# Performance work log

Measured on AMD Instinct MI355X. Metric: run time of the kernel, lower is better.

## Reference

```python
import jax, jax.numpy as jnp
import numpy as np

N = 65536   # base nodes
M = 65536   # union local nodes
E = 1048576 # base edges
EL = 1048576 # local edges
K = 131072  # membership entries
F = 128     # in_channels
H = 128     # hidden_dim
L = 2       # num_layers
OUT = 2
ALPHA = 0.9


def setup_inputs() -> dict:
    key = jax.random.key(0)
    ks = jax.random.split(key, 16)
    s = 1.0 / np.sqrt(H)
    return {
        "x": jax.random.normal(ks[0], (N, F), jnp.float32),
        "edge_index": jax.random.randint(ks[1], (2, E), 0, N, jnp.int64 if jax.config.jax_enable_x64 else jnp.int32),
        "edge_weight": jax.random.uniform(ks[2], (E,), jnp.float32),
        "local_x0": jax.random.normal(ks[3], (M, F), jnp.float32),
        "copy2orig": jax.random.randint(ks[4], (M,), 0, N),
        "local_adj_index": jax.random.randint(ks[5], (2, EL), 0, M),
        "local_adj_value": jax.random.uniform(ks[6], (EL,), jnp.float32),
        "memb_idx": jax.random.randint(ks[7], (K,), 0, M),
        "memb_gid": jax.random.randint(ks[8], (K,), 0, 64),
        "B": 64,
        "Wb_in": jax.random.normal(ks[9], (F, H), jnp.float32) * s,
        "bb_in": jnp.zeros((H,), jnp.float32),
        "Wl_in": jax.random.normal(ks[10], (F, H), jnp.float32) * s,
        "bl_in": jnp.zeros((H,), jnp.float32),
        "W_base": jax.random.normal(ks[11], (L, H, H), jnp.float32) * s,
        "b_base": jnp.zeros((L, H), jnp.float32),
        "W_local": jax.random.normal(ks[12], (L, H, H), jnp.float32) * s,
        "b_local": jnp.zeros((L, H), jnp.float32),
        "Wp": jax.random.normal(ks[13], (H, OUT), jnp.float32) * s,
        "bp": jnp.zeros((OUT,), jnp.float32),
    }


def reference(x, edge_index, edge_weight, local_x0, copy2orig, local_adj_index,
              local_adj_value, memb_idx, memb_gid, B, Wb_in, bb_in, Wl_in, bl_in,
              W_base, b_base, W_local, b_local, Wp, bp):
    n = x.shape[0]
    m = local_x0.shape[0]
    # input projections (dropout is identity in eval mode)
    base_x = jax.nn.relu(x @ Wb_in + bb_in)
    local_x = jax.nn.relu(local_x0 @ Wl_in + bl_in)
    src, dst = edge_index[0], edge_index[1]
    lsrc, ldst = local_adj_index[0], local_adj_index[1]
    for l in range(W_base.shape[0]):
        # base graph propagation: normalized-adjacency spmm then linear+relu
        base_agg = jax.ops.segment_sum(base_x[src] * edge_weight[:, None], dst, num_segments=n)
        base_x = jax.nn.relu(base_agg @ W_base[l] + b_base[l])
        # local union-graph propagation + alpha-mix with base features via copy2orig
        local_agg = jax.ops.segment_sum(local_x[lsrc] * local_adj_value[:, None], ldst, num_segments=m)
        mix = ALPHA * local_agg + (1.0 - ALPHA) * base_x[copy2orig]
        local_x = jax.nn.relu(mix @ W_local[l] + b_local[l])
    # scatter-mean pooling by membership (fused sum + count)
    sub = jax.ops.segment_sum(local_x[memb_idx], memb_gid, num_segments=B)
    cnt = jax.ops.segment_sum(jnp.ones((memb_gid.shape[0], 1), local_x.dtype), memb_gid, num_segments=B)
    sub = sub / jnp.maximum(cnt, 1.0)
    return sub @ Wp + bp
```

## Files before the change

kernel.cpp:

```cpp
#include <hip/hip_runtime.h>

typedef __attribute__((ext_vector_type(8))) short bfrag;
typedef __attribute__((ext_vector_type(4))) float ffrag;

__device__ __forceinline__ ushort f2bf(float f) {
    union { float f; unsigned u; } v{f};
    unsigned r = v.u + 0x7fff + ((v.u >> 16) & 1);
    return (ushort)(r >> 16);
}
__device__ __forceinline__ float bf2f(ushort u) {
    union { unsigned u; float f; } v{(unsigned)u << 16};
    return v.f;
}
__device__ __forceinline__ float bflo(unsigned u) {
    union { unsigned u; float f; } v{u << 16};
    return v.f;
}
__device__ __forceinline__ float bfhi(unsigned u) {
    union { unsigned u; float f; } v{u & 0xffff0000u};
    return v.f;
}

#define WDEC (1.f / 65535.f)

#define NB 512
#define BSH 7
#define CH2 2048
#define CAP 4608
#define PCAP 2432


__global__ __launch_bounds__(256) void wprep_zero(const float* __restrict__ Wb_in, const float* __restrict__ Wl_in,
                                                  const float* __restrict__ W_base, const float* __restrict__ W_local,
                                                  ushort* __restrict__ out,
                                                  int* __restrict__ bs_cur, int* __restrict__ ls_cur,
                                                  int* __restrict__ p_cur, int* __restrict__ psum) {
    const int bid = blockIdx.x;
    const int t = threadIdx.x;
    if (bid < 384) {
        int idx = bid * 256 + t;
        int mat = idx >> 14;
        int i = idx & 16383;
        int nn = i >> 7, kk = i & 127;
        const float* src;
        switch (mat) {
            case 0: src = Wb_in; break;
            case 1: src = Wl_in; break;
            case 2: src = W_base; break;
            case 3: src = W_base + 16384; break;
            case 4: src = W_local; break;
            default: src = W_local + 16384; break;
        }
        out[(size_t)mat * 16384 + i] = f2bf(src[kk * 128 + nn]);
    } else {
        int i = (bid - 384) * 256 + t;
        if (i < 512) { bs_cur[i] = i * CAP; ls_cur[i] = i * CAP; }
        if (i < 64) p_cur[i] = i * PCAP;
        psum[i] = 0;
    }
}


__global__ __launch_bounds__(512) void b1p(const int* __restrict__ b_src, const int* __restrict__ b_dst,
                                           const float* __restrict__ b_w, int* __restrict__ b_cur,
                                           int2* __restrict__ b_staged,
                                           const int* __restrict__ l_src, const int* __restrict__ l_dst,
                                           const float* __restrict__ l_w, int* __restrict__ l_cur,
                                           int2* __restrict__ l_staged,
                                           const int* __restrict__ memb_idx, const int* __restrict__ memb_gid,
                                           int* __restrict__ p_cursor, int* __restrict__ p_sorted) {
    __shared__ int cnt_s[NB], base_l[NB], base_g[NB], curs[NB];
    __shared__ int wtot[8];
    __shared__ int2 stage[CH2];
    __shared__ ushort bb[CH2];
    __shared__ int lhist[64], lbase[64], loff[1024];
    const int t = threadIdx.x;
    const int bid = blockIdx.x;
    if (bid < 1024) {
        const int g = bid >> 9;
        const int* src = g ? l_src : b_src;
        const int* dst = g ? l_dst : b_dst;
        const float* w = g ? l_w : b_w;
        int* bcursor = g ? l_cur : b_cur;
        int2* staged = g ? l_staged : b_staged;
        const int base = (bid & 511) * CH2;
        cnt_s[t] = 0;
        __syncthreads();
#pragma unroll
        for (int u = 0; u < CH2 / 512; ++u) {
            int b = ((unsigned)dst[base + u * 512 + t]) >> BSH;
            atomicAdd(&cnt_s[b], 1);
        }
        __syncthreads();
        int v = cnt_s[t];
        int lane = t & 63, wid = t >> 6;
        int inc = v;
        for (int o = 1; o < 64; o <<= 1) { int x = __shfl_up(inc, o); if (lane >= o) inc += x; }
        if (lane == 63) wtot[wid] = inc;
        __syncthreads();
        int wpre = 0;
#pragma unroll
        for (int j = 0; j < 8; ++j) if (j < wid) wpre += wtot[j];
        int excl = wpre + inc - v;
        base_l[t] = excl;
        curs[t] = excl;
        base_g[t] = atomicAdd(&bcursor[t], v);
        __syncthreads();
#pragma unroll
        for (int u = 0; u < CH2 / 512; ++u) {
            int e = base + u * 512 + t;
            int d = dst[e];
            int b = ((unsigned)d) >> BSH;
            int p = atomicAdd(&curs[b], 1);
            stage[p] = make_int2((src[e] & 0xffff) | ((d & 127) << 16), __float_as_int(w[e]));
            bb[p] = (ushort)b;
        }
        __syncthreads();
        for (int i = t; i < CH2; i += 512) {
            int b = bb[i];
            staged[base_g[b] + (i - base_l[b])] = stage[i];
        }
    } else {
        if (t < 64) lhist[t] = 0;
        __syncthreads();
        const int base = (bid - 1024) * 1024;
        int g[2], ix[2];
#pragma unroll
        for (int u = 0; u < 2; ++u) {
            int e = base + u * 512 + t;
            g[u] = memb_gid[e];
            ix[u] = memb_idx[e];
            loff[u * 512 + t] = atomicAdd(&lhist[g[u]], 1);
        }
        __syncthreads();
        if (t < 64) lbase[t] = atomicAdd(&p_cursor[t], lhist[t]);
        __syncthreads();
#pragma unroll
        for (int u = 0; u < 2; ++u) {
            int pos = lbase[g[u]] + loff[u * 512 + t];
            p_sorted[pos] = ix[u];
        }
    }
}

#define ASTRIDE 136


__global__ __launch_bounds__(256) void b2g(const int* __restrict__ b_cur, const int2* __restrict__ b_staged,
                                           int2* __restrict__ b_rng, int* __restrict__ b_edges,
                                           const int* __restrict__ l_cur, const int2* __restrict__ l_staged,
                                           int2* __restrict__ l_rng, int* __restrict__ l_edges,
                                           const float* __restrict__ Ab, const float* __restrict__ Al,
                                           const ushort* __restrict__ Wt,
                                           const float* __restrict__ biasb, const float* __restrict__ biasl,
                                           ushort* __restrict__ Yb, ushort* __restrict__ Yl) {
    __shared__ __align__(16) char smem[52224];
    __shared__ int cnt[256], curs[256], wt4[4];
    const int t = threadIdx.x;
    const int bid = blockIdx.x;
    if (bid < 1024) {
        const int g = bid >> 9;
        const int b = bid & 511;
        const int* bcur = g ? l_cur : b_cur;
        const int2* staged = g ? l_staged : b_staged;
        int2* rng = g ? l_rng : b_rng;
        int* edges = g ? l_edges : b_edges;
        const int s0 = b * CAP;
        int len = bcur[b] - s0;
        if (len > CAP) len = CAP;
        cnt[t] = 0;
        __syncthreads();
        int* seg = (int*)smem;
        int* ord = (int*)(smem + CAP * 4);
        unsigned char* segd = (unsigned char*)(smem + CAP * 8);
        for (int i = t; i < len; i += 256) {
            int2 se = staged[s0 + i];
            int key = (((se.x >> 16) & 127) << 1) | ((se.x >> 15) & 1);
            unsigned wq = (unsigned)(__int_as_float(se.y) * 65535.f + 0.5f);
            seg[i] = (int)(((unsigned)se.x & 0xffffu) | (wq << 16));
            segd[i] = (unsigned char)key;
            atomicAdd(&cnt[key], 1);
        }
        __syncthreads();
        int v = cnt[t];
        int lane = t & 63, wid = t >> 6;
        int inc = v;
        for (int o = 1; o < 64; o <<= 1) { int x = __shfl_up(inc, o); if (lane >= o) inc += x; }
        if (lane == 63) wt4[wid] = inc;
        __syncthreads();
        int wpre = 0;
#pragma unroll
        for (int j = 0; j < 4; ++j) if (j < wid) wpre += wt4[j];
        int excl = wpre + inc - v;
        curs[t] = excl;
        if (!(t & 1))
            rng[b * 128 + (t >> 1)] = make_int2(s0 + excl, s0 + excl + v + cnt[t + 1]);
        __syncthreads();
        for (int i = t; i < len; i += 256) {
            int p = atomicAdd(&curs[segd[i]], 1);
            ord[p] = seg[i];
        }
        __syncthreads();
        for (int i = t; i < len; i += 256)
            edges[s0 + i] = ord[i];
    } else {
        ushort* As = (ushort*)smem;
        ushort* Bs = (ushort*)(smem + 64 * ASTRIDE * 2);
        const int bid2 = bid - 1024;
        const int g = bid2 >> 10;
        const float* A = g ? Al : Ab;
        const ushort* W = Wt + (size_t)g * 16384;
        const float* bias = g ? biasl : biasb;
        ushort* Y = g ? Yl : Yb;
        const int r0 = (bid2 & 1023) * 64;

#pragma unroll
        for (int p = 0; p < 8; ++p) {
            int c = p * 256 + t;
            int row = c >> 5, o4 = (c & 31) * 4;
            float4 v = *(const float4*)(A + (size_t)(r0 + row) * 128 + o4);
            ushort4 u;
            u.x = f2bf(v.x); u.y = f2bf(v.y); u.z = f2bf(v.z); u.w = f2bf(v.w);
            *(ushort4*)&As[row * ASTRIDE + o4] = u;
        }
#pragma unroll
        for (int p = 0; p < 8; ++p) {
            int c = p * 256 + t;
            int n = c >> 4, o8 = (c & 15) * 8;
            *(uint4*)&Bs[n * ASTRIDE + o8] = *(const uint4*)(W + n * 128 + o8);
        }
        __syncthreads();

        const int lane = t & 63;
        const int w = t >> 6;
        const int wm = (w & 1) * 32;
        const int wn = (w >> 1) * 64;
        const int q = lane >> 4;
        const int l16 = lane & 15;

        ffrag acc[2][4];
#pragma unroll
        for (int mt = 0; mt < 2; ++mt)
#pragma unroll
            for (int nt = 0; nt < 4; ++nt) acc[mt][nt] = (ffrag){0.f, 0.f, 0.f, 0.f};

#pragma unroll
        for (int kc = 0; kc < 4; ++kc) {
            bfrag a[2], b[4];
#pragma unroll
            for (int mt = 0; mt < 2; ++mt)
                a[mt] = *(const bfrag*)&As[(wm + mt * 16 + l16) * ASTRIDE + kc * 32 + q * 8];
#pragma unroll
            for (int nt = 0; nt < 4; ++nt)
                b[nt] = *(const bfrag*)&Bs[(wn + nt * 16 + l16) * ASTRIDE + kc * 32 + q * 8];
#pragma unroll
            for (int mt = 0; mt < 2; ++mt)
#pragma unroll
                for (int nt = 0; nt < 4; ++nt)
                    acc[mt][nt] = __builtin_amdgcn_mfma_f32_16x16x32_bf16(a[mt], b[nt], acc[mt][nt], 0, 0, 0);
        }

        float bias_v[4];
#pragma unroll
        for (int nt = 0; nt < 4; ++nt) bias_v[nt] = bias[wn + nt * 16 + l16];
#pragma unroll
        for (int mt = 0; mt < 2; ++mt)
#pragma unroll
            for (int nt = 0; nt < 4; ++nt)
#pragma unroll
                for (int r = 0; r < 4; ++r) {
                    int row = r0 + wm + mt * 16 + q * 4 + r;
                    int col = wn + nt * 16 + l16;
                    float v = fmaxf(acc[mt][nt][r] + bias_v[nt], 0.f);
                    Y[(size_t)row * 128 + col] = f2bf(v);
                }
    }
}


template <bool MIX>
__global__ __launch_bounds__(256) void gemm_layer(const ushort* __restrict__ A, const ushort* __restrict__ A2,
                                                  const int* __restrict__ ridx,
                                                  const ushort* __restrict__ Wt, const float* __restrict__ bias,
                                                  ushort* __restrict__ Y) {
    __shared__ ushort As[64 * ASTRIDE];
    __shared__ ushort Bs[128 * ASTRIDE];
    const int tid = threadIdx.x;
    const int r0 = blockIdx.x * 64;

#pragma unroll
    for (int p = 0; p < 4; ++p) {
        int c = p * 256 + tid;
        int row = c >> 4, o8 = (c & 15) * 8;
        uint4 v = *(const uint4*)(A + (size_t)(r0 + row) * 128 + o8);
        if (MIX) {
            int rr = ridx[r0 + row];
            uint4 v2 = *(const uint4*)(A2 + (size_t)rr * 128 + o8);
            uint4 o;
            float x0, x1;
            x0 = 0.9f * bflo(v.x) + 0.1f * bflo(v2.x);
            x1 = 0.9f * bfhi(v.x) + 0.1f * bfhi(v2.x);
            o.x = (unsigned)f2bf(x0) | ((unsigned)f2bf(x1) << 16);
            x0 = 0.9f * bflo(v.y) + 0.1f * bflo(v2.y);
            x1 = 0.9f * bfhi(v.y) + 0.1f * bfhi(v2.y);
            o.y = (unsigned)f2bf(x0) | ((unsigned)f2bf(x1) << 16);
            x0 = 0.9f * bflo(v.z) + 0.1f * bflo(v2.z);
            x1 = 0.9f * bfhi(v.z) + 0.1f * bfhi(v2.z);
            o.z = (unsigned)f2bf(x0) | ((unsigned)f2bf(x1) << 16);
            x0 = 0.9f * bflo(v.w) + 0.1f * bflo(v2.w);
            x1 = 0.9f * bfhi(v.w) + 0.1f * bfhi(v2.w);
            o.w = (unsigned)f2bf(x0) | ((unsigned)f2bf(x1) << 16);
            v = o;
        }
        *(uint4*)&As[row * ASTRIDE + o8] = v;
    }
#pragma unroll
    for (int p = 0; p < 8; ++p) {
        int c = p * 256 + tid;
        int n = c >> 4, o8 = (c & 15) * 8;
        *(uint4*)&Bs[n * ASTRIDE + o8] = *(const uint4*)(Wt + n * 128 + o8);
    }
    __syncthreads();

    const int lane = tid & 63;
    const int w = tid >> 6;
    const int wm = (w & 1) * 32;
    const int wn = (w >> 1) * 64;
    const int q = lane >> 4;
    const int l16 = lane & 15;

    ffrag acc[2][4];
#pragma unroll
    for (int mt = 0; mt < 2; ++mt)
#pragma unroll
        for (int nt = 0; nt < 4; ++nt) acc[mt][nt] = (ffrag){0.f, 0.f, 0.f, 0.f};

#pragma unroll
    for (int kc = 0; kc < 4; ++kc) {
        bfrag a[2], b[4];
#pragma unroll
        for (int mt = 0; mt < 2; ++mt)
            a[mt] = *(const bfrag*)&As[(wm + mt * 16 + l16) * ASTRIDE + kc * 32 + q * 8];
#pragma unroll
        for (int nt = 0; nt < 4; ++nt)
            b[nt] = *(const bfrag*)&Bs[(wn + nt * 16 + l16) * ASTRIDE + kc * 32 + q * 8];
#pragma unroll
        for (int mt = 0; mt < 2; ++mt)
#pragma unroll
            for (int nt = 0; nt < 4; ++nt)
                acc[mt][nt] = __builtin_amdgcn_mfma_f32_16x16x32_bf16(a[mt], b[nt], acc[mt][nt], 0, 0, 0);
    }

    float bias_v[4];
#pragma unroll
    for (int nt = 0; nt < 4; ++nt) bias_v[nt] = bias[wn + nt * 16 + l16];
#pragma unroll
    for (int mt = 0; mt < 2; ++mt)
#pragma unroll
        for (int nt = 0; nt < 4; ++nt)
#pragma unroll
            for (int r = 0; r < 4; ++r) {
                int row = r0 + wm + mt * 16 + q * 4 + r;
                int col = wn + nt * 16 + l16;
                float v = fmaxf(acc[mt][nt][r] + bias_v[nt], 0.f);
                Y[(size_t)row * 128 + col] = f2bf(v);
            }
}


__global__ __launch_bounds__(256) void spmm2(const int2* __restrict__ bs_rng, const int* __restrict__ bs_edges,
                                             const ushort* __restrict__ Xb, ushort* __restrict__ Yb,
                                             const int2* __restrict__ ls_rng, const int* __restrict__ ls_edges,
                                             const ushort* __restrict__ Xl, ushort* __restrict__ Yl) {
    const int g = blockIdx.x & 1;
    const int2* rng = g ? ls_rng : bs_rng;
    const int* edges = g ? ls_edges : bs_edges;
    const ushort* X = g ? Xl : Xb;
    ushort* Y = g ? Yl : Yb;
    int node = (((blockIdx.x >> 1) * 256) + threadIdx.x) >> 5;
    int lane = threadIdx.x & 31;
    int2 r = rng[node];
    int s0 = r.x;
    int s1 = r.y;
    const int f = lane * 4;
    float a0 = 0.f, a1 = 0.f, a2 = 0.f, a3 = 0.f;
    int e = s0;
    for (; e < s1 && (e & 3); ++e) {
        unsigned pe = (unsigned)edges[e];
        float w = (float)(pe >> 16) * WDEC;
        ushort4 v = *(const ushort4*)(X + ((size_t)(pe & 0xffffu) << 7) + f);
        a0 += w * bf2f(v.x); a1 += w * bf2f(v.y); a2 += w * bf2f(v.z); a3 += w * bf2f(v.w);
    }
    for (; e + 8 <= s1; e += 8) {
        int4 pA = *(const int4*)(edges + e);
        int4 pB = *(const int4*)(edges + e + 4);
        ushort4 v0 = *(const ushort4*)(X + ((size_t)((unsigned)pA.x & 0xffffu) << 7) + f);
        ushort4 v1 = *(const ushort4*)(X + ((size_t)((unsigned)pA.y & 0xffffu) << 7) + f);
        ushort4 v2 = *(const ushort4*)(X + ((size_t)((unsigned)pA.z & 0xffffu) << 7) + f);
        ushort4 v3 = *(const ushort4*)(X + ((size_t)((unsigned)pA.w & 0xffffu) << 7) + f);
        ushort4 v4 = *(const ushort4*)(X + ((size_t)((unsigned)pB.x & 0xffffu) << 7) + f);
        ushort4 v5 = *(const ushort4*)(X + ((size_t)((unsigned)pB.y & 0xffffu) << 7) + f);
        ushort4 v6 = *(const ushort4*)(X + ((size_t)((unsigned)pB.z & 0xffffu) << 7) + f);
        ushort4 v7 = *(const ushort4*)(X + ((size_t)((unsigned)pB.w & 0xffffu) << 7) + f);
        float w0 = (float)((unsigned)pA.x >> 16) * WDEC;
        float w1 = (float)((unsigned)pA.y >> 16) * WDEC;
        float w2 = (float)((unsigned)pA.z >> 16) * WDEC;
        float w3 = (float)((unsigned)pA.w >> 16) * WDEC;
        float w4 = (float)((unsigned)pB.x >> 16) * WDEC;
        float w5 = (float)((unsigned)pB.y >> 16) * WDEC;
        float w6 = (float)((unsigned)pB.z >> 16) * WDEC;
        float w7 = (float)((unsigned)pB.w >> 16) * WDEC;
        a0 += w0 * bf2f(v0.x) + w1 * bf2f(v1.x) + w2 * bf2f(v2.x) + w3 * bf2f(v3.x)
            + w4 * bf2f(v4.x) + w5 * bf2f(v5.x) + w6 * bf2f(v6.x) + w7 * bf2f(v7.x);
        a1 += w0 * bf2f(v0.y) + w1 * bf2f(v1.y) + w2 * bf2f(v2.y) + w3 * bf2f(v3.y)
            + w4 * bf2f(v4.y) + w5 * bf2f(v5.y) + w6 * bf2f(v6.y) + w7 * bf2f(v7.y);
        a2 += w0 * bf2f(v0.z) + w1 * bf2f(v1.z) + w2 * bf2f(v2.z) + w3 * bf2f(v3.z)
            + w4 * bf2f(v4.z) + w5 * bf2f(v5.z) + w6 * bf2f(v6.z) + w7 * bf2f(v7.z);
        a3 += w0 * bf2f(v0.w) + w1 * bf2f(v1.w) + w2 * bf2f(v2.w) + w3 * bf2f(v3.w)
            + w4 * bf2f(v4.w) + w5 * bf2f(v5.w) + w6 * bf2f(v6.w) + w7 * bf2f(v7.w);
    }
    for (; e + 4 <= s1; e += 4) {
        int4 pA = *(const int4*)(edges + e);
        ushort4 v0 = *(const ushort4*)(X + ((size_t)((unsigned)pA.x & 0xffffu) << 7) + f);
        ushort4 v1 = *(const ushort4*)(X + ((size_t)((unsigned)pA.y & 0xffffu) << 7) + f);
        ushort4 v2 = *(const ushort4*)(X + ((size_t)((unsigned)pA.z & 0xffffu) << 7) + f);
        ushort4 v3 = *(const ushort4*)(X + ((size_t)((unsigned)pA.w & 0xffffu) << 7) + f);
        float w0 = (float)((unsigned)pA.x >> 16) * WDEC;
        float w1 = (float)((unsigned)pA.y >> 16) * WDEC;
        float w2 = (float)((unsigned)pA.z >> 16) * WDEC;
        float w3 = (float)((unsigned)pA.w >> 16) * WDEC;
        a0 += w0 * bf2f(v0.x) + w1 * bf2f(v1.x) + w2 * bf2f(v2.x) + w3 * bf2f(v3.x);
        a1 += w0 * bf2f(v0.y) + w1 * bf2f(v1.y) + w2 * bf2f(v2.y) + w3 * bf2f(v3.y);
        a2 += w0 * bf2f(v0.z) + w1 * bf2f(v1.z) + w2 * bf2f(v2.z) + w3 * bf2f(v3.z);
        a3 += w0 * bf2f(v0.w) + w1 * bf2f(v1.w) + w2 * bf2f(v2.w) + w3 * bf2f(v3.w);
    }
    for (; e < s1; ++e) {
        unsigned pe = (unsigned)edges[e];
        float w = (float)(pe >> 16) * WDEC;
        ushort4 v = *(const ushort4*)(X + ((size_t)(pe & 0xffffu) << 7) + f);
        a0 += w * bf2f(v.x); a1 += w * bf2f(v.y); a2 += w * bf2f(v.z); a3 += w * bf2f(v.w);
    }
    ushort4 o;
    o.x = f2bf(a0);
    o.y = f2bf(a1);
    o.z = f2bf(a2);
    o.w = f2bf(a3);
    *(ushort4*)(Y + (size_t)node * 128 + f) = o;
}


__global__ __launch_bounds__(256) void pool_accum(const int* __restrict__ p_cur, const int* __restrict__ sorted_idx,
                                                  const ushort* __restrict__ X, float* __restrict__ gsum) {
    const int g = blockIdx.x >> 5;
    const int sgm = blockIdx.x & 31;
    const int gs = g * PCAP;
    const int cnt = p_cur[g] - gs;
    const int e_begin = gs + ((cnt * sgm) >> 5);
    const int e_end = gs + ((cnt * (sgm + 1)) >> 5);
    const int t = threadIdx.x;
    const int fp = t & 63;
    const int sub = t >> 6;
    float ax = 0.f, ay = 0.f;
#pragma unroll 4
    for (int e = e_begin + sub; e < e_end; e += 4) {
        int idx = sorted_idx[e];
        ushort2 u = *(const ushort2*)(X + (size_t)idx * 128 + fp * 2);
        ax += bf2f(u.x);
        ay += bf2f(u.y);
    }
    __shared__ float sx[256], sy[256];
    sx[t] = ax;
    sy[t] = ay;
    __syncthreads();
    if (t < 64) {
        atomicAdd(&gsum[g * 128 + fp * 2 + 0], sx[t] + sx[t + 64] + sx[t + 128] + sx[t + 192]);
        atomicAdd(&gsum[g * 128 + fp * 2 + 1], sy[t] + sy[t + 64] + sy[t + 128] + sy[t + 192]);
    }
}


__global__ __launch_bounds__(128) void final_kernel(const float* __restrict__ gsum, const int* __restrict__ p_cur,
                                                    const float* __restrict__ Wp, const float* __restrict__ bp,
                                                    float* __restrict__ out) {
    int t = threadIdx.x;
    int g = t >> 1;
    int o = t & 1;
    float cnt = (float)(p_cur[g] - g * PCAP);
    float inv = 1.f / fmaxf(cnt, 1.f);
    float acc = bp[o];
    for (int f = 0; f < 128; ++f) acc += gsum[g * 128 + f] * inv * Wp[f * 2 + o];
    out[g * 2 + o] = acc;
}


extern "C" void kernel_launch(void* const* d_in, const int* in_sizes, int n_in,
                              void* d_out, int out_size, void* d_ws, size_t ws_size,
                              hipStream_t stream) {
    const float* x              = (const float*)d_in[0];
    const int*   edge_index     = (const int*)d_in[1];
    const float* edge_weight    = (const float*)d_in[2];
    const float* local_x0       = (const float*)d_in[3];
    const int*   copy2orig      = (const int*)d_in[4];
    const int*   local_adj_idx  = (const int*)d_in[5];
    const float* local_adj_val  = (const float*)d_in[6];
    const int*   memb_idx       = (const int*)d_in[7];
    const int*   memb_gid       = (const int*)d_in[8];
    const float* Wb_in          = (const float*)d_in[10];
    const float* bb_in          = (const float*)d_in[11];
    const float* Wl_in          = (const float*)d_in[12];
    const float* bl_in          = (const float*)d_in[13];
    const float* W_base         = (const float*)d_in[14];
    const float* b_base         = (const float*)d_in[15];
    const float* W_local        = (const float*)d_in[16];
    const float* b_local        = (const float*)d_in[17];
    const float* Wp             = (const float*)d_in[18];
    const float* bp             = (const float*)d_in[19];
    float* out = (float*)d_out;

    constexpr int N = 65536, M = 65536, E = 1048576, EL = 1048576, K = 131072, H = 128;

    char* wsb = (char*)d_ws;
    size_t off = 0;
    auto alloc = [&](size_t bytes) -> char* {
        char* p = wsb + off;
        off += (bytes + 255) & ~(size_t)255;
        return p;
    };
    int2*   bs_rng   = (int2*)alloc((size_t)N * 8);
    int*    bs_edges = (int*)alloc((size_t)NB * CAP * 4);
    int2*   bs_stage = (int2*)alloc((size_t)NB * CAP * 8);
    int*    bs_cur   = (int*)alloc(NB * 4);
    int2*   ls_rng   = (int2*)alloc((size_t)M * 8);
    int*    ls_edges = (int*)alloc((size_t)NB * CAP * 4);
    int2*   ls_stage = (int2*)alloc((size_t)NB * CAP * 8);
    int*    ls_cur   = (int*)alloc(NB * 4);
    ushort* bufA     = (ushort*)alloc((size_t)N * H * 2);
    ushort* bufB     = (ushort*)alloc((size_t)M * H * 2);
    ushort* bufC     = (ushort*)alloc((size_t)N * H * 2);
    ushort* bufD     = (ushort*)alloc((size_t)M * H * 2);
    ushort* wt       = (ushort*)alloc((size_t)6 * 16384 * 2);
    int*    p_cursor = (int*)alloc(64 * 4);
    int*    p_sorted = (int*)alloc((size_t)64 * PCAP * 4);
    float*  pool_sum = (float*)alloc(64 * 128 * 4);

    const int* b_src = edge_index;
    const int* b_dst = edge_index + E;
    const int* l_src = local_adj_idx;
    const int* l_dst = local_adj_idx + EL;

    wprep_zero<<<416, 256, 0, stream>>>(Wb_in, Wl_in, W_base, W_local, wt,
                                        bs_cur, ls_cur, p_cursor, (int*)pool_sum);

    b1p<<<1152, 512, 0, stream>>>(b_src, b_dst, edge_weight, bs_cur, bs_stage,
                                  l_src, l_dst, local_adj_val, ls_cur, ls_stage,
                                  memb_idx, memb_gid, p_cursor, p_sorted);

    b2g<<<3072, 256, 0, stream>>>(bs_cur, bs_stage, bs_rng, bs_edges,
                                  ls_cur, ls_stage, ls_rng, ls_edges,
                                  x, local_x0, wt, bb_in, bl_in, bufA, bufB);

    for (int l = 0; l < 2; ++l) {
        spmm2<<<16384, 256, 0, stream>>>(bs_rng, bs_edges, bufA, bufC,
                                         ls_rng, ls_edges, bufB, bufD);
        gemm_layer<false><<<N / 64, 256, 0, stream>>>(bufC, nullptr, nullptr,
                                                      wt + (size_t)(2 + l) * 16384, b_base + (size_t)l * H, bufA);
        gemm_layer<true><<<M / 64, 256, 0, stream>>>(bufD, bufA, copy2orig,
                                                     wt + (size_t)(4 + l) * 16384, b_local + (size_t)l * H, bufB);
    }

    pool_accum<<<64 * 32, 256, 0, stream>>>(p_cursor, p_sorted, bufB, pool_sum);
    final_kernel<<<1, 128, 0, stream>>>(pool_sum, p_cursor, Wp, bp, out);
}
```

Measured before the change: 392.9 us.

## Pack staged edges into 32-bit words with 9-bit weights; prefetch edge indices in SpMM

Edge weights are now quantized to 9 bits at the staging pass, so each staged edge fits in one 32-bit word holding the source id, the low destination bits and the weight. This halves staging traffic and simplifies the per-bucket sort to 128 keys with one range per row instead of paired keys. The SpMM 8-edge loop is software-pipelined, loading the next edge-index vectors before processing the current ones, with padding added to the edge buffers to allow the lookahead reads. Quantizing weights to 9 bits lowers precision noticeably compared with the previous 16-bit encoding and may cost accuracy.

```diff
diff --git a/kernel.cpp b/kernel.cpp
--- a/kernel.cpp
+++ b/kernel.cpp
@@ -21,7 +21,7 @@
     return v.f;
 }
 
-#define WDEC (1.f / 65535.f)
+#define WDEC (1.f / 511.f)
 
 #define NB 512
 #define BSH 7
@@ -63,15 +63,15 @@
 
 __global__ __launch_bounds__(512) void b1p(const int* __restrict__ b_src, const int* __restrict__ b_dst,
                                            const float* __restrict__ b_w, int* __restrict__ b_cur,
-                                           int2* __restrict__ b_staged,
+                                           int* __restrict__ b_staged,
                                            const int* __restrict__ l_src, const int* __restrict__ l_dst,
                                            const float* __restrict__ l_w, int* __restrict__ l_cur,
-                                           int2* __restrict__ l_staged,
+                                           int* __restrict__ l_staged,
                                            const int* __restrict__ memb_idx, const int* __restrict__ memb_gid,
                                            int* __restrict__ p_cursor, int* __restrict__ p_sorted) {
     __shared__ int cnt_s[NB], base_l[NB], base_g[NB], curs[NB];
     __shared__ int wtot[8];
-    __shared__ int2 stage[CH2];
+    __shared__ int stage[CH2];
     __shared__ ushort bb[CH2];
     __shared__ int lhist[64], lbase[64], loff[1024];
     const int t = threadIdx.x;
@@ -82,7 +82,7 @@
         const int* dst = g ? l_dst : b_dst;
         const float* w = g ? l_w : b_w;
         int* bcursor = g ? l_cur : b_cur;
-        int2* staged = g ? l_staged : b_staged;
+        int* staged = g ? l_staged : b_staged;
         const int base = (bid & 511) * CH2;
         cnt_s[t] = 0;
         __syncthreads();
@@ -112,7 +112,8 @@
             int d = dst[e];
             int b = ((unsigned)d) >> BSH;
             int p = atomicAdd(&curs[b], 1);
-            stage[p] = make_int2((src[e] & 0xffff) | ((d & 127) << 16), __float_as_int(w[e]));
+            unsigned wq = (unsigned)(w[e] * 511.f + 0.5f);
+            stage[p] = (int)(((unsigned)src[e] & 0xffffu) | ((unsigned)(d & 127) << 16) | (wq << 23));
             bb[p] = (ushort)b;
         }
         __syncthreads();
@@ -146,55 +147,55 @@
 #define ASTRIDE 136
 
 
-__global__ __launch_bounds__(256) void b2g(const int* __restrict__ b_cur, const int2* __restrict__ b_staged,
+__global__ __launch_bounds__(256) void b2g(const int* __restrict__ b_cur, const int* __restrict__ b_staged,
                                            int2* __restrict__ b_rng, int* __restrict__ b_edges,
-                                           const int* __restrict__ l_cur, const int2* __restrict__ l_staged,
+                                           const int* __restrict__ l_cur, const int* __restrict__ l_staged,
                                            int2* __restrict__ l_rng, int* __restrict__ l_edges,
                                            const float* __restrict__ Ab, const float* __restrict__ Al,
                                            const ushort* __restrict__ Wt,
                                            const float* __restrict__ biasb, const float* __restrict__ biasl,
                                            ushort* __restrict__ Yb, ushort* __restrict__ Yl) {
     __shared__ __align__(16) char smem[52224];
-    __shared__ int cnt[256], curs[256], wt4[4];
+    __shared__ int cnt[128], curs[128], wt2[2];
     const int t = threadIdx.x;
     const int bid = blockIdx.x;
     if (bid < 1024) {
         const int g = bid >> 9;
         const int b = bid & 511;
         const int* bcur = g ? l_cur : b_cur;
-        const int2* staged = g ? l_staged : b_staged;
+        const int* staged = g ? l_staged : b_staged;
         int2* rng = g ? l_rng : b_rng;
         int* edges = g ? l_edges : b_edges;
         const int s0 = b * CAP;
         int len = bcur[b] - s0;
         if (len > CAP) len = CAP;
-        cnt[t] = 0;
+        if (t < 128) cnt[t] = 0;
         __syncthreads();
         int* seg = (int*)smem;
         int* ord = (int*)(smem + CAP * 4);
         unsigned char* segd = (unsigned char*)(smem + CAP * 8);
         for (int i = t; i < len; i += 256) {
-            int2 se = staged[s0 + i];
-            int key = (((se.x >> 16) & 127) << 1) | ((se.x >> 15) & 1);
-            unsigned wq = (unsigned)(__int_as_float(se.y) * 65535.f + 0.5f);
-            seg[i] = (int)(((unsigned)se.x & 0xffffu) | (wq << 16));
-            segd[i] = (unsigned char)key;
-            atomicAdd(&cnt[key], 1);
-        }
-        __syncthreads();
-        int v = cnt[t];
-        int lane = t & 63, wid = t >> 6;
-        int inc = v;
-        for (int o = 1; o < 64; o <<= 1) { int x = __shfl_up(inc, o); if (lane >= o) inc += x; }
-        if (lane == 63) wt4[wid] = inc;
-        __syncthreads();
-        int wpre = 0;
-#pragma unroll
-        for (int j = 0; j < 4; ++j) if (j < wid) wpre += wt4[j];
-        int excl = wpre + inc - v;
-        curs[t] = excl;
-        if (!(t & 1))
-            rng[b * 128 + (t >> 1)] = make_int2(s0 + excl, s0 + excl + v + cnt[t + 1]);
+            int v = staged[s0 + i];
+            int dl = (v >> 16) & 127;
+            unsigned wq = ((unsigned)v) >> 23;
+            seg[i] = (int)(((unsigned)v & 0xffffu) | (wq << 16));
+            segd[i] = (unsigned char)dl;
+            atomicAdd(&cnt[dl], 1);
+        }
+        __syncthreads();
+        int v = 0, inc = 0;
+        if (t < 128) {
+            v = cnt[t];
+            inc = v;
+            for (int o = 1; o < 64; o <<= 1) { int x = __shfl_up(inc, o); if ((t & 63) >= o) inc += x; }
+            if ((t & 63) == 63) wt2[t >> 6] = inc;
+        }
+        __syncthreads();
+        if (t < 128) {
+            int excl = inc - v + (t >= 64 ? wt2[0] : 0);
+            curs[t] = excl;
+            rng[b * 128 + t] = make_int2(s0 + excl, s0 + excl + v);
+        }
         __syncthreads();
         for (int i = t; i < len; i += 256) {
             int p = atomicAdd(&curs[segd[i]], 1);
@@ -368,6 +369,34 @@
 }
 
 
+#define PROC8(pA, pB)                                                                          \
+    {                                                                                          \
+        ushort4 v0 = *(const ushort4*)(X + ((size_t)((unsigned)pA.x & 0xffffu) << 7) + f);     \
+        ushort4 v1 = *(const ushort4*)(X + ((size_t)((unsigned)pA.y & 0xffffu) << 7) + f);     \
+        ushort4 v2 = *(const ushort4*)(X + ((size_t)((unsigned)pA.z & 0xffffu) << 7) + f);     \
+        ushort4 v3 = *(const ushort4*)(X + ((size_t)((unsigned)pA.w & 0xffffu) << 7) + f);     \
+        ushort4 v4 = *(const ushort4*)(X + ((size_t)((unsigned)pB.x & 0xffffu) << 7) + f);     \
+        ushort4 v5 = *(const ushort4*)(X + ((size_t)((unsigned)pB.y & 0xffffu) << 7) + f);     \
+        ushort4 v6 = *(const ushort4*)(X + ((size_t)((unsigned)pB.z & 0xffffu) << 7) + f);     \
+        ushort4 v7 = *(const ushort4*)(X + ((size_t)((unsigned)pB.w & 0xffffu) << 7) + f);     \
+        float w0 = (float)((unsigned)pA.x >> 16) * WDEC;                                       \
+        float w1 = (float)((unsigned)pA.y >> 16) * WDEC;                                       \
+        float w2 = (float)((unsigned)pA.z >> 16) * WDEC;                                       \
+        float w3 = (float)((unsigned)pA.w >> 16) * WDEC;                                       \
+        float w4 = (float)((unsigned)pB.x >> 16) * WDEC;                                       \
+        float w5 = (float)((unsigned)pB.y >> 16) * WDEC;                                       \
+        float w6 = (float)((unsigned)pB.z >> 16) * WDEC;                                       \
+        float w7 = (float)((unsigned)pB.w >> 16) * WDEC;                                       \
+        a0 += w0 * bf2f(v0.x) + w1 * bf2f(v1.x) + w2 * bf2f(v2.x) + w3 * bf2f(v3.x)            \
+            + w4 * bf2f(v4.x) + w5 * bf2f(v5.x) + w6 * bf2f(v6.x) + w7 * bf2f(v7.x);           \
+        a1 += w0 * bf2f(v0.y) + w1 * bf2f(v1.y) + w2 * bf2f(v2.y) + w3 * bf2f(v3.y)            \
+            + w4 * bf2f(v4.y) + w5 * bf2f(v5.y) + w6 * bf2f(v6.y) + w7 * bf2f(v7.y);           \
+        a2 += w0 * bf2f(v0.z) + w1 * bf2f(v1.z) + w2 * bf2f(v2.z) + w3 * bf2f(v3.z)            \
+            + w4 * bf2f(v4.z) + w5 * bf2f(v5.z) + w6 * bf2f(v6.z) + w7 * bf2f(v7.z);           \
+        a3 += w0 * bf2f(v0.w) + w1 * bf2f(v1.w) + w2 * bf2f(v2.w) + w3 * bf2f(v3.w)            \
+            + w4 * bf2f(v4.w) + w5 * bf2f(v5.w) + w6 * bf2f(v6.w) + w7 * bf2f(v7.w);           \
+    }
+
 __global__ __launch_bounds__(256) void spmm2(const int2* __restrict__ bs_rng, const int* __restrict__ bs_edges,
                                              const ushort* __restrict__ Xb, ushort* __restrict__ Yb,
                                              const int2* __restrict__ ls_rng, const int* __restrict__ ls_edges,
@@ -391,33 +420,18 @@
         ushort4 v = *(const ushort4*)(X + ((size_t)(pe & 0xffffu) << 7) + f);
         a0 += w * bf2f(v.x); a1 += w * bf2f(v.y); a2 += w * bf2f(v.z); a3 += w * bf2f(v.w);
     }
-    for (; e + 8 <= s1; e += 8) {
+    if (e + 8 <= s1) {
         int4 pA = *(const int4*)(edges + e);
         int4 pB = *(const int4*)(edges + e + 4);
-        ushort4 v0 = *(const ushort4*)(X + ((size_t)((unsigned)pA.x & 0xffffu) << 7) + f);
-        ushort4 v1 = *(const ushort4*)(X + ((size_t)((unsigned)pA.y & 0xffffu) << 7) + f);
-        ushort4 v2 = *(const ushort4*)(X + ((size_t)((unsigned)pA.z & 0xffffu) << 7) + f);
-        ushort4 v3 = *(const ushort4*)(X + ((size_t)((unsigned)pA.w & 0xffffu) << 7) + f);
-        ushort4 v4 = *(const ushort4*)(X + ((size_t)((unsigned)pB.x & 0xffffu) << 7) + f);
-        ushort4 v5 = *(const ushort4*)(X + ((size_t)((unsigned)pB.y & 0xffffu) << 7) + f);
-        ushort4 v6 = *(const ushort4*)(X + ((size_t)((unsigned)pB.z & 0xffffu) << 7) + f);
-        ushort4 v7 = *(const ushort4*)(X + ((size_t)((unsigned)pB.w & 0xffffu) << 7) + f);
-        float w0 = (float)((unsigned)pA.x >> 16) * WDEC;
-        float w1 = (float)((unsigned)pA.y >> 16) * WDEC;
-        float w2 = (float)((unsigned)pA.z >> 16) * WDEC;
-        float w3 = (float)((unsigned)pA.w >> 16) * WDEC;
-        float w4 = (float)((unsigned)pB.x >> 16) * WDEC;
-        float w5 = (float)((unsigned)pB.y >> 16) * WDEC;
-        float w6 = (float)((unsigned)pB.z >> 16) * WDEC;
-        float w7 = (float)((unsigned)pB.w >> 16) * WDEC;
-        a0 += w0 * bf2f(v0.x) + w1 * bf2f(v1.x) + w2 * bf2f(v2.x) + w3 * bf2f(v3.x)
-            + w4 * bf2f(v4.x) + w5 * bf2f(v5.x) + w6 * bf2f(v6.x) + w7 * bf2f(v7.x);
-        a1 += w0 * bf2f(v0.y) + w1 * bf2f(v1.y) + w2 * bf2f(v2.y) + w3 * bf2f(v3.y)
-            + w4 * bf2f(v4.y) + w5 * bf2f(v5.y) + w6 * bf2f(v6.y) + w7 * bf2f(v7.y);
-        a2 += w0 * bf2f(v0.z) + w1 * bf2f(v1.z) + w2 * bf2f(v2.z) + w3 * bf2f(v3.z)
-            + w4 * bf2f(v4.z) + w5 * bf2f(v5.z) + w6 * bf2f(v6.z) + w7 * bf2f(v7.z);
-        a3 += w0 * bf2f(v0.w) + w1 * bf2f(v1.w) + w2 * bf2f(v2.w) + w3 * bf2f(v3.w)
-            + w4 * bf2f(v4.w) + w5 * bf2f(v5.w) + w6 * bf2f(v6.w) + w7 * bf2f(v7.w);
+        for (; e + 16 <= s1; e += 8) {
+            int4 nA = *(const int4*)(edges + e + 8);
+            int4 nB = *(const int4*)(edges + e + 12);
+            PROC8(pA, pB);
+            pA = nA;
+            pB = nB;
+        }
+        PROC8(pA, pB);
+        e += 8;
     }
     for (; e + 4 <= s1; e += 4) {
         int4 pA = *(const int4*)(edges + e);
@@ -527,12 +541,12 @@
         return p;
     };
     int2*   bs_rng   = (int2*)alloc((size_t)N * 8);
-    int*    bs_edges = (int*)alloc((size_t)NB * CAP * 4);
-    int2*   bs_stage = (int2*)alloc((size_t)NB * CAP * 8);
+    int*    bs_edges = (int*)alloc((size_t)NB * CAP * 4 + 64);
+    int*    bs_stage = (int*)alloc((size_t)NB * CAP * 4);
     int*    bs_cur   = (int*)alloc(NB * 4);
     int2*   ls_rng   = (int2*)alloc((size_t)M * 8);
-    int*    ls_edges = (int*)alloc((size_t)NB * CAP * 4);
-    int2*   ls_stage = (int2*)alloc((size_t)NB * CAP * 8);
+    int*    ls_edges = (int*)alloc((size_t)NB * CAP * 4 + 64);
+    int*    ls_stage = (int*)alloc((size_t)NB * CAP * 4);
     int*    ls_cur   = (int*)alloc(NB * 4);
     ushort* bufA     = (ushort*)alloc((size_t)N * H * 2);
     ushort* bufB     = (ushort*)alloc((size_t)M * H * 2);
```

After: 386.9 us (median of 2 runs). About the same (-1.5%).
